# Performance work log

Hardware: AMD Instinct MI355X
Metric: run time of the kernel (lower is better)

## Reference

```python
import jax, jax.numpy as jnp
import numpy as np

TEMPERATURE = 0.1
NSAMPLE = 32
B, N_PER, M_PER, C_FEAT = 2, 16384, 4096, 64


def setup_inputs() -> dict:
    key = jax.random.key(0)
    ks = jax.random.split(key, 4)
    xyz = jax.random.normal(ks[0], (B * N_PER, 3), jnp.float32)
    new_xyz = jax.random.normal(ks[1], (B * M_PER, 3), jnp.float32)
    new_xyz_r = jax.random.uniform(ks[2], (B * M_PER, 1), jnp.float32, minval=0.5, maxval=1.0)
    features = jax.random.normal(ks[3], (B * N_PER, C_FEAT), jnp.float32)
    xyz_batch_cnt = jnp.full((B,), N_PER, jnp.int32)
    new_xyz_batch_cnt = jnp.full((B,), M_PER, jnp.int32)
    temperature_decay = jnp.ones((1,), jnp.float32)
    return dict(xyz=xyz, xyz_batch_cnt=xyz_batch_cnt, new_xyz=new_xyz,
                new_xyz_r=new_xyz_r, new_xyz_batch_cnt=new_xyz_batch_cnt,
                features=features, temperature_decay=temperature_decay)


def _ball_query(xyz_b, new_xyz_b, r_b, nsample):
    # xyz_b: (B,N,3), new_xyz_b: (B,M,3), r_b: (B,M)
    # Returns idx (B,M,nsample) int32 (batch-local point indices, first-in-order
    # within the ball, remaining slots filled with first hit, 0 if empty) and
    # empty mask (B,M) bool. Mirrors the CUDA ball_query_deform kernel.
    N = xyz_b.shape[1]
    d2 = jnp.sum((new_xyz_b[:, :, None, :] - xyz_b[:, None, :, :]) ** 2, axis=-1)  # (B,M,N)
    within = d2 < (r_b ** 2)[..., None]
    # key = point index if within radius else N; top_k of -key gives the first
    # nsample in-ball indices in ascending index order.
    key = jnp.where(within, jnp.arange(N, dtype=jnp.int32), jnp.int32(N))
    neg_vals, _ = jax.lax.top_k(-key, nsample)
    cand = -neg_vals  # (B,M,nsample)
    cnt = within.sum(axis=-1)  # (B,M)
    slot_valid = jnp.arange(nsample) < cnt[..., None]
    idx = jnp.where(slot_valid, cand, cand[..., :1])  # pad with first found index
    empty = cnt == 0
    idx = jnp.where(empty[..., None], 0, idx)
    return idx.astype(jnp.int32), empty


def reference(xyz, xyz_batch_cnt, new_xyz, new_xyz_r, new_xyz_batch_cnt, features, temperature_decay):
    b = xyz_batch_cnt.shape[0]
    n = xyz.shape[0] // b
    m = new_xyz.shape[0] // b
    c = features.shape[1]
    real_t = TEMPERATURE * temperature_decay[0]
    explore_r = new_xyz_r + real_t * 5.0  # (M_tot, 1)

    xyz_b = xyz.reshape(b, n, 3)
    nxyz_b = new_xyz.reshape(b, m, 3)
    idx_b, empty_b = _ball_query(xyz_b, nxyz_b, explore_r.reshape(b, m), NSAMPLE)

    gather = jax.vmap(lambda pts, i: pts[i])  # per-batch gather

    grouped_xyz = gather(xyz_b, idx_b)                 # (B,M,ns,3)
    grouped_xyz = grouped_xyz - nxyz_b[:, :, None, :]  # center
    grouped_xyz = jnp.where(empty_b[:, :, None, None], 0.0, grouped_xyz)
    grouped_xyz = grouped_xyz.reshape(b * m, NSAMPLE, 3).transpose(0, 2, 1)  # (M_tot,3,ns)

    dist_xyz = jnp.sqrt(jnp.sum(grouped_xyz * grouped_xyz, axis=1))  # (M_tot,ns)
    weights = 1.0 - jax.nn.sigmoid((dist_xyz - new_xyz_r) / real_t)  # (M_tot,ns)

    feat_b = features.reshape(b, n, c)
    grouped_feat = gather(feat_b, idx_b)  # (B,M,ns,C)
    grouped_feat = jnp.where(empty_b[:, :, None, None], 0.0, grouped_feat)
    grouped_feat = grouped_feat.reshape(b * m, NSAMPLE, c).transpose(0, 2, 1)  # (M_tot,C,ns)

    new_features = jnp.concatenate([grouped_xyz, grouped_feat], axis=1)  # (M_tot,3+C,ns)
    idx = idx_b.reshape(b * m, NSAMPLE)
    return new_features, weights, idx
```

## Files before the change

kernel.cpp:

```cpp
#include <hip/hip_runtime.h>
#include <math.h>

#define NS 32
#define WPB 4
#define SCAN0 2048
#define TSTRIDE 36

__device__ __forceinline__ void write_query(
    int m, int bb, bool empty, int lane,
    const int* sIdxW, float* sT,
    const float* __restrict__ xyz, const float* __restrict__ new_xyz,
    const float* __restrict__ new_xyz_r, const float* __restrict__ features,
    float real_t, float* __restrict__ out, int N_per, int C, int M_tot)
{
#pragma clang fp contract(off)
    const float* xb = xyz + (size_t)bb * N_per * 3;
    const int    j  = lane & 31;
    const size_t nf_base = (size_t)m * (3 + C) * NS;
    float* wout = out + (size_t)M_tot * (3 + C) * NS;
    float* iout = wout + (size_t)M_tot * NS;

    if (lane < NS) {
        const float qx = new_xyz[(size_t)m * 3 + 0];
        const float qy = new_xyz[(size_t)m * 3 + 1];
        const float qz = new_xyz[(size_t)m * 3 + 2];
        const float r_orig = new_xyz_r[m];
        const int pj = empty ? 0 : sIdxW[j];
        float gx = 0.f, gy = 0.f, gz = 0.f;
        if (!empty) {
            gx = xb[(size_t)pj * 3 + 0] - qx;
            gy = xb[(size_t)pj * 3 + 1] - qy;
            gz = xb[(size_t)pj * 3 + 2] - qz;
        }
        float d2 = gx * gx;
        d2 = d2 + gy * gy;
        d2 = d2 + gz * gz;
        float dist = sqrtf(d2);
        float wt = 1.0f / (1.0f + expf((dist - r_orig) / real_t));
        out[nf_base + 0 * NS + j] = gx;
        out[nf_base + 1 * NS + j] = gy;
        out[nf_base + 2 * NS + j] = gz;
        wout[(size_t)m * NS + j] = wt;
        iout[(size_t)m * NS + j] = (float)pj;
    }

    const float* fb = features + (size_t)bb * N_per * C;
    int c0 = 0;
    for (; c0 + 32 <= C; c0 += 32) {
        const int k  = lane & 7;
        const int f4 = 4 * (k & 3);
        #pragma unroll
        for (int t = 0; t < 4; ++t) {
            const int r  = 8 * t + (lane >> 3);
            const int pj = empty ? 0 : sIdxW[r];
            float4 v = make_float4(0.f, 0.f, 0.f, 0.f);
            if (!empty) v = *(const float4*)(fb + (size_t)pj * C + c0 + 4 * k);
            const int rs = r ^ f4;
            sT[(4 * k + 0) * TSTRIDE + rs] = v.x;
            sT[(4 * k + 1) * TSTRIDE + rs] = v.y;
            sT[(4 * k + 2) * TSTRIDE + rs] = v.z;
            sT[(4 * k + 3) * TSTRIDE + rs] = v.w;
        }
        const int jg = lane & 7;
        #pragma unroll
        for (int s2 = 0; s2 < 4; ++s2) {
            const int ch = 8 * s2 + (lane >> 3);
            const int jb = (4 * jg) ^ (4 * ((ch >> 2) & 3));
            float4 w = *(const float4*)&sT[ch * TSTRIDE + jb];
            *(float4*)&out[nf_base + (size_t)(3 + c0 + ch) * NS + 4 * jg] = w;
        }
    }
    if (c0 < C) {
        const int h  = lane >> 5;
        const int pj = empty ? 0 : sIdxW[j];
        const float* frow = fb + (size_t)pj * C;
        for (int c = c0 + h; c < C; c += 2) {
            float v = empty ? 0.f : frow[c];
            out[nf_base + (size_t)(3 + c) * NS + j] = v;
        }
    }
}

__device__ __forceinline__ int scan_range(
    const float* __restrict__ xb, float qx, float qy, float qz, float er2,
    int rb, int re, int lane, unsigned long long lt, int* hits)
{
#pragma clang fp contract(off)
    int cnt = 0;
    for (int base = rb; base < re; base += 256) {
        float d2k[4];
        #pragma unroll
        for (int k = 0; k < 4; ++k) {
            int p = base + k * 64 + lane;
            int pc = (p < re) ? p : (re - 1);
            const float* pp = xb + (size_t)pc * 3;
            float dx = pp[0] - qx, dy = pp[1] - qy, dz = pp[2] - qz;
            float d2 = dx * dx;
            d2 = d2 + dy * dy;
            d2 = d2 + dz * dz;
            d2k[k] = (p < re) ? d2 : 1e30f;
        }
        #pragma unroll
        for (int k = 0; k < 4; ++k) {
            bool hit = d2k[k] < er2;
            unsigned long long msk = __ballot(hit);
            if (hit) {
                int slot = cnt + (int)__popcll(msk & lt);
                if (slot < NS) hits[slot] = base + k * 64 + lane;
            }
            cnt += (int)__popcll(msk);
        }
        if (cnt >= NS) break;
    }
    return cnt;
}

__global__ __launch_bounds__(256) void qgd_F(
    const float* __restrict__ xyz, const float* __restrict__ new_xyz,
    const float* __restrict__ new_xyz_r, const float* __restrict__ features,
    const float* __restrict__ tdec, float* __restrict__ out,
    int N_per, int M_per, int C, int M_tot)
{
#pragma clang fp contract(off)
    __shared__ __align__(16) float sBuf[WPB * 32 * TSTRIDE];
    __shared__ int sIdx[WPB][NS];
    __shared__ int sH[WPB][NS];
    __shared__ int sCnt[WPB];
    __shared__ int sStrag[WPB];
    __shared__ int sC[WPB];
    __shared__ int sM[NS];
    __shared__ int sTot;

    const int lane = threadIdx.x & 63;
    const int wv   = threadIdx.x >> 6;
    const int m    = blockIdx.x * WPB + wv;
    const bool valid = (m < M_tot);

    const float real_t = 0.1f * tdec[0];
    const unsigned long long lt = (1ull << lane) - 1ull;
    const int scan0 = (SCAN0 < N_per) ? SCAN0 : N_per;

    int cnt = 0;
    int bb = 0;
    if (valid) {
        bb = m / M_per;
        const float* xb = xyz + (size_t)bb * N_per * 3;
        const float qx = new_xyz[(size_t)m * 3 + 0];
        const float qy = new_xyz[(size_t)m * 3 + 1];
        const float qz = new_xyz[(size_t)m * 3 + 2];
        const float er  = new_xyz_r[m] + real_t * 5.0f;
        const float er2 = er * er;

        cnt = scan_range(xb, qx, qy, qz, er2, 0, scan0, lane, lt, sIdx[wv]);

        if (cnt >= NS) {
            write_query(m, bb, false, lane, sIdx[wv],
                        sBuf + wv * (32 * TSTRIDE),
                        xyz, new_xyz, new_xyz_r, features, real_t, out,
                        N_per, C, M_tot);
        }
    }
    if (lane == 0) {
        sCnt[wv]   = cnt;
        sStrag[wv] = (valid && cnt < NS) ? 1 : 0;
    }
    __syncthreads();

    for (int s = 0; s < WPB; ++s) {
        if (!sStrag[s]) continue;

        const int ms  = blockIdx.x * WPB + s;
        const int bbs = ms / M_per;
        const float* xbs = xyz + (size_t)bbs * N_per * 3;
        const float qx = new_xyz[(size_t)ms * 3 + 0];
        const float qy = new_xyz[(size_t)ms * 3 + 1];
        const float qz = new_xyz[(size_t)ms * 3 + 2];
        const float er  = new_xyz_r[ms] + real_t * 5.0f;
        const float er2 = er * er;

        const int rem = N_per - scan0;
        const int rb  = scan0 + (int)(((long long)rem * wv) / WPB);
        const int re  = scan0 + (int)(((long long)rem * (wv + 1)) / WPB);

        int c2 = scan_range(xbs, qx, qy, qz, er2, rb, re, lane, lt, sH[wv]);
        if (lane == 0) sC[wv] = (c2 < NS) ? c2 : NS;
        __syncthreads();

        if (threadIdx.x < NS) {
            const int j  = threadIdx.x;
            const int cp = sCnt[s];
            const int c0 = sC[0], c1 = sC[1], c2_ = sC[2], c3 = sC[3];
            const int o0 = cp, o1 = o0 + c0, o2 = o1 + c1, o3 = o2 + c2_;
            const int tot = o3 + c3;
            int v = 0;
            if (j < tot) {
                if      (j <  o0) v = sIdx[s][j];
                else if (j <  o1) v = sH[0][j - o0];
                else if (j <  o2) v = sH[1][j - o1];
                else if (j <  o3) v = sH[2][j - o2];
                else              v = sH[3][j - o3];
            }
            int first = 0;
            if      (cp  > 0) first = sIdx[s][0];
            else if (c0  > 0) first = sH[0][0];
            else if (c1  > 0) first = sH[1][0];
            else if (c2_ > 0) first = sH[2][0];
            else if (c3  > 0) first = sH[3][0];
            sM[j] = (tot == 0) ? 0 : ((j < tot) ? v : first);
            if (j == 0) sTot = tot;
        }
        __syncthreads();

        if (wv == 0) {
            write_query(ms, bbs, (sTot == 0), lane, sM, sBuf,
                        xyz, new_xyz, new_xyz_r, features, real_t, out,
                        N_per, C, M_tot);
        }
        __syncthreads();
    }
}

extern "C" void kernel_launch(void* const* d_in, const int* in_sizes, int n_in,
                              void* d_out, int out_size, void* d_ws, size_t ws_size,
                              hipStream_t stream) {
    const float* xyz       = (const float*)d_in[0];
    const float* new_xyz   = (const float*)d_in[2];
    const float* new_xyz_r = (const float*)d_in[3];
    const float* features  = (const float*)d_in[5];
    const float* tdec      = (const float*)d_in[6];

    const int B     = in_sizes[1];
    const int N_tot = in_sizes[0] / 3;
    const int M_tot = in_sizes[2] / 3;
    const int C     = in_sizes[5] / N_tot;
    const int N_per = N_tot / B;
    const int M_per = M_tot / B;

    float* out = (float*)d_out;

    const int blocks = (M_tot + WPB - 1) / WPB;
    qgd_F<<<blocks, 256, 0, stream>>>(xyz, new_xyz, new_xyz_r, features,
                                      tdec, out, N_per, M_per, C, M_tot);
}
```

Baseline: 115.7 us.

## Use persistent grid with global work queue for straggler queries

Replaces the per-block straggler handling with a persistent-style kernel: each block first runs the fast prefix scan for a strided set of query groups and pushes unresolved queries onto a global atomic list. Blocks then pop straggler queries from the shared queue and rescan the full point range cooperatively with all four waves. This aims to balance the expensive straggler work across the whole GPU instead of serializing it inside the block that found it. In exchange it adds two memsets, global atomics and a spin-wait that depends on all producer blocks being resident or finishing. It also rescans the first 2048 points for stragglers, repeating part of the earlier scan.

Result: slower. 427.9 us (+269.9%).

```diff
diff --git a/kernel.cpp b/kernel.cpp
--- a/kernel.cpp
+++ b/kernel.cpp
@@ -5,6 +5,7 @@
 #define WPB 4
 #define SCAN0 2048
 #define TSTRIDE 36
+#define MAXBLK 2048
 
 __device__ __forceinline__ void write_query(
     int m, int bb, bool empty, int lane,
@@ -115,94 +116,117 @@
     return cnt;
 }
 
-__global__ __launch_bounds__(256) void qgd_F(
+__global__ __launch_bounds__(256, 8) void qgd_W(
     const float* __restrict__ xyz, const float* __restrict__ new_xyz,
     const float* __restrict__ new_xyz_r, const float* __restrict__ features,
     const float* __restrict__ tdec, float* __restrict__ out,
+    int* __restrict__ ws,
     int N_per, int M_per, int C, int M_tot)
 {
 #pragma clang fp contract(off)
     __shared__ __align__(16) float sBuf[WPB * 32 * TSTRIDE];
     __shared__ int sIdx[WPB][NS];
     __shared__ int sH[WPB][NS];
-    __shared__ int sCnt[WPB];
-    __shared__ int sStrag[WPB];
     __shared__ int sC[WPB];
     __shared__ int sM[NS];
     __shared__ int sTot;
+    __shared__ int sMq;
+
+    int* push = ws + 0;
+    int* pop  = ws + 1;
+    int* done = ws + 2;
+    int* list = ws + 4;
 
     const int lane = threadIdx.x & 63;
     const int wv   = threadIdx.x >> 6;
-    const int m    = blockIdx.x * WPB + wv;
-    const bool valid = (m < M_tot);
-
+    const unsigned long long lt = (1ull << lane) - 1ull;
     const float real_t = 0.1f * tdec[0];
-    const unsigned long long lt = (1ull << lane) - 1ull;
     const int scan0 = (SCAN0 < N_per) ? SCAN0 : N_per;
-
-    int cnt = 0;
-    int bb = 0;
-    if (valid) {
-        bb = m / M_per;
-        const float* xb = xyz + (size_t)bb * N_per * 3;
-        const float qx = new_xyz[(size_t)m * 3 + 0];
-        const float qy = new_xyz[(size_t)m * 3 + 1];
-        const float qz = new_xyz[(size_t)m * 3 + 2];
-        const float er  = new_xyz_r[m] + real_t * 5.0f;
+    const int ngroups = (M_tot + WPB - 1) / WPB;
+
+    for (int g = blockIdx.x; g < ngroups; g += gridDim.x) {
+        const int m = g * WPB + wv;
+        if (m < M_tot) {
+            const int bb = m / M_per;
+            const float* xb = xyz + (size_t)bb * N_per * 3;
+            const float qx = new_xyz[(size_t)m * 3 + 0];
+            const float qy = new_xyz[(size_t)m * 3 + 1];
+            const float qz = new_xyz[(size_t)m * 3 + 2];
+            const float er  = new_xyz_r[m] + real_t * 5.0f;
+            const float er2 = er * er;
+
+            int cnt = scan_range(xb, qx, qy, qz, er2, 0, scan0, lane, lt,
+                                 sIdx[wv]);
+            if (cnt >= NS) {
+                write_query(m, bb, false, lane, sIdx[wv],
+                            sBuf + wv * (32 * TSTRIDE),
+                            xyz, new_xyz, new_xyz_r, features, real_t, out,
+                            N_per, C, M_tot);
+            } else if (lane == 0) {
+                int pos = atomicAdd(push, 1);
+                atomicExch(&list[pos], m);
+            }
+        }
+    }
+    __syncthreads();
+    if (threadIdx.x == 0) {
+        __threadfence();
+        atomicAdd(done, 1);
+    }
+
+    const int nprod = gridDim.x;
+    for (;;) {
+        if (threadIdx.x == 0) {
+            int mq = -1;
+            int i = atomicAdd(pop, 1);
+            if (i >= M_tot) {
+                mq = -1;
+            } else {
+                for (;;) {
+                    mq = atomicAdd(&list[i], 0);
+                    if (mq >= 0) break;
+                    int d = atomicAdd(done, 0);
+                    if (d >= nprod) {
+                        int p = atomicAdd(push, 0);
+                        if (i >= p) { mq = -1; break; }
+                    }
+                    __builtin_amdgcn_s_sleep(8);
+                }
+            }
+            sMq = mq;
+        }
+        __syncthreads();
+        const int mq = sMq;
+        if (mq < 0) break;
+
+        const int bbs = mq / M_per;
+        const float* xbs = xyz + (size_t)bbs * N_per * 3;
+        const float qx = new_xyz[(size_t)mq * 3 + 0];
+        const float qy = new_xyz[(size_t)mq * 3 + 1];
+        const float qz = new_xyz[(size_t)mq * 3 + 2];
+        const float er  = new_xyz_r[mq] + real_t * 5.0f;
         const float er2 = er * er;
 
-        cnt = scan_range(xb, qx, qy, qz, er2, 0, scan0, lane, lt, sIdx[wv]);
-
-        if (cnt >= NS) {
-            write_query(m, bb, false, lane, sIdx[wv],
-                        sBuf + wv * (32 * TSTRIDE),
-                        xyz, new_xyz, new_xyz_r, features, real_t, out,
-                        N_per, C, M_tot);
-        }
-    }
-    if (lane == 0) {
-        sCnt[wv]   = cnt;
-        sStrag[wv] = (valid && cnt < NS) ? 1 : 0;
-    }
-    __syncthreads();
-
-    for (int s = 0; s < WPB; ++s) {
-        if (!sStrag[s]) continue;
-
-        const int ms  = blockIdx.x * WPB + s;
-        const int bbs = ms / M_per;
-        const float* xbs = xyz + (size_t)bbs * N_per * 3;
-        const float qx = new_xyz[(size_t)ms * 3 + 0];
-        const float qy = new_xyz[(size_t)ms * 3 + 1];
-        const float qz = new_xyz[(size_t)ms * 3 + 2];
-        const float er  = new_xyz_r[ms] + real_t * 5.0f;
-        const float er2 = er * er;
-
-        const int rem = N_per - scan0;
-        const int rb  = scan0 + (int)(((long long)rem * wv) / WPB);
-        const int re  = scan0 + (int)(((long long)rem * (wv + 1)) / WPB);
-
+        const int rb = (int)(((long long)N_per * wv) / WPB);
+        const int re = (int)(((long long)N_per * (wv + 1)) / WPB);
         int c2 = scan_range(xbs, qx, qy, qz, er2, rb, re, lane, lt, sH[wv]);
         if (lane == 0) sC[wv] = (c2 < NS) ? c2 : NS;
         __syncthreads();
 
         if (threadIdx.x < NS) {
             const int j  = threadIdx.x;
-            const int cp = sCnt[s];
             const int c0 = sC[0], c1 = sC[1], c2_ = sC[2], c3 = sC[3];
-            const int o0 = cp, o1 = o0 + c0, o2 = o1 + c1, o3 = o2 + c2_;
+            const int o1 = c0, o2 = c0 + c1, o3 = o2 + c2_;
             const int tot = o3 + c3;
             int v = 0;
             if (j < tot) {
-                if      (j <  o0) v = sIdx[s][j];
-                else if (j <  o1) v = sH[0][j - o0];
-                else if (j <  o2) v = sH[1][j - o1];
-                else if (j <  o3) v = sH[2][j - o2];
-                else              v = sH[3][j - o3];
+                if      (j >= o3) v = sH[3][j - o3];
+                else if (j >= o2) v = sH[2][j - o2];
+                else if (j >= o1) v = sH[1][j - o1];
+                else              v = sH[0][j];
             }
             int first = 0;
-            if      (cp  > 0) first = sIdx[s][0];
-            else if (c0  > 0) first = sH[0][0];
+            if      (c0  > 0) first = sH[0][0];
             else if (c1  > 0) first = sH[1][0];
             else if (c2_ > 0) first = sH[2][0];
             else if (c3  > 0) first = sH[3][0];
@@ -212,11 +236,10 @@
         __syncthreads();
 
         if (wv == 0) {
-            write_query(ms, bbs, (sTot == 0), lane, sM, sBuf,
+            write_query(mq, bbs, (sTot == 0), lane, sM, sBuf,
                         xyz, new_xyz, new_xyz_r, features, real_t, out,
                         N_per, C, M_tot);
         }
-        __syncthreads();
     }
 }
 
@@ -237,8 +260,14 @@
     const int M_per = M_tot / B;
 
     float* out = (float*)d_out;
-
-    const int blocks = (M_tot + WPB - 1) / WPB;
-    qgd_F<<<blocks, 256, 0, stream>>>(xyz, new_xyz, new_xyz_r, features,
-                                      tdec, out, N_per, M_per, C, M_tot);
-}
+    int*   ws  = (int*)d_ws;
+
+    hipMemsetAsync(ws, 0, 16, stream);
+    hipMemsetAsync(ws + 4, 0xFF, (size_t)M_tot * sizeof(int), stream);
+
+    const int ngroups = (M_tot + WPB - 1) / WPB;
+    const int blocks  = (ngroups < MAXBLK) ? ngroups : MAXBLK;
+    qgd_W<<<blocks, 256, 0, stream>>>(xyz, new_xyz, new_xyz_r, features,
+                                      tdec, out, ws,
+                                      N_per, M_per, C, M_tot);
+}
```
